# Performance work log

Measured on AMD Instinct MI355X. Metric: run time of the kernel, lower is better.

Reference implementation:

```python
import jax, jax.numpy as jnp
import numpy as np

N_EMBD = 1024
HEAD_SIZE = 64
B, T = 8, 2048


def setup_inputs() -> dict:
    key = jax.random.key(0)
    k1, k2, k3, k4 = jax.random.split(key, 4)
    scale = 1.0 / np.sqrt(N_EMBD)
    return {
        "x": jax.random.normal(k1, (B, T, N_EMBD), dtype=jnp.float32),
        "Wq": jax.random.normal(k2, (N_EMBD, HEAD_SIZE), dtype=jnp.float32) * scale,
        "Wk": jax.random.normal(k3, (N_EMBD, HEAD_SIZE), dtype=jnp.float32) * scale,
        "Wv": jax.random.normal(k4, (N_EMBD, HEAD_SIZE), dtype=jnp.float32) * scale,
    }


def reference(x, Wq, Wk, Wv):
    # x: [B, T, C]; projections (no bias)
    q = jnp.einsum("btc,ch->bth", x, Wq)
    k = jnp.einsum("btc,ch->bth", x, Wk)
    v = jnp.einsum("btc,ch->bth", x, Wv)
    head_size = k.shape[-1]
    # scaled scores [B, T, T]
    wei = jnp.einsum("bth,bsh->bts", q, k) * (head_size ** -0.5)
    # causal mask (lower-triangular keeps)
    Tlen = x.shape[1]
    causal = jnp.tril(jnp.ones((Tlen, Tlen), dtype=bool))
    wei = jnp.where(causal[None, :, :], wei, -jnp.inf)
    wei = jax.nn.softmax(wei, axis=-1)
    # dropout p=0 (eval) -> identity
    out = jnp.einsum("bts,bsh->bth", wei, v)
    return out
```

## Files before the change

### kernel.cpp

```cpp
#include <hip/hip_runtime.h>
#include <hip/hip_bf16.h>
#include <math.h>

#define Bn 8
#define Tn 2048
#define Cn 1024
#define Hn 64

typedef __attribute__((ext_vector_type(8))) short short8;
typedef __attribute__((ext_vector_type(4))) float floatx4;

#define ATTN_SCALE 0.18033688011112042f

__device__ inline unsigned short f2bf(float f) {
    union { float f; unsigned int u; } x; x.f = f;
    unsigned int r = x.u + 0x7fffu + ((x.u >> 16) & 1u);
    return (unsigned short)(r >> 16);
}

__device__ inline uint2 pack4bf(float4 v) {
    __hip_bfloat162 lo = __float22bfloat162_rn(make_float2(v.x, v.y));
    __hip_bfloat162 hi = __float22bfloat162_rn(make_float2(v.z, v.w));
    uint2 r;
    r.x = *reinterpret_cast<unsigned int*>(&lo);
    r.y = *reinterpret_cast<unsigned int*>(&hi);
    return r;
}

__device__ inline float rsum16(float v) {
    v += __shfl_xor(v, 1);
    v += __shfl_xor(v, 2);
    v += __shfl_xor(v, 4);
    v += __shfl_xor(v, 8);
    return v;
}

__global__ __launch_bounds__(256) void prep_w(
    const float* __restrict__ Wq, const float* __restrict__ Wk,
    const float* __restrict__ Wv, unsigned short* __restrict__ Wfrag)
{
    const int gid = blockIdx.x * 256 + threadIdx.x;
    const int c    = gid >> 11;
    const int rem  = gid & 2047;
    const int ks   = rem >> 6;
    const int lane = rem & 63;
    const int ln = lane & 15, qd = lane >> 4;
    const int mat = c >> 2, nc = c & 3;
    const float* W = (mat == 0) ? Wq : (mat == 1) ? Wk : Wv;
    const float sc = (mat == 0) ? ATTN_SCALE : 1.0f;
    const int col = nc * 16 + ln;
    unsigned short o[8];
    #pragma unroll
    for (int j = 0; j < 8; ++j)
        o[j] = f2bf(W[(size_t)(ks * 32 + qd * 8 + j) * Hn + col] * sc);
    *reinterpret_cast<short8*>(Wfrag + (size_t)gid * 8) = *reinterpret_cast<short8*>(o);
}

__global__ __launch_bounds__(256, 4) void proj_mfma(
    const float* __restrict__ x, const unsigned short* __restrict__ Wfrag,
    unsigned short* __restrict__ qbf, unsigned short* __restrict__ kfrag,
    unsigned short* __restrict__ vfrag)
{
    __shared__ unsigned short xs[32 * 512];

    const int ln   = threadIdx.x & 15;
    const int quad = (threadIdx.x >> 4) & 3;
    const int w    = threadIdx.x >> 6;
    const int lane = threadIdx.x & 63;
    const int row0 = blockIdx.x * 16;

    const int srow = threadIdx.x >> 4;
    const int sf   = threadIdx.x & 15;
    const float4* xrow4 = reinterpret_cast<const float4*>(x + (size_t)(row0 + srow) * Cn);

    float4 ld[16];
    #pragma unroll
    for (int it = 0; it < 16; ++it)
        ld[it] = xrow4[sf + 16 * it];
    #pragma unroll
    for (int it = 0; it < 16; ++it) {
        const int f4g = sf + 16 * it;
        const int s = f4g >> 3;
        const int q = (f4g >> 1) & 3;
        const int j = (f4g & 1) * 4;
        *reinterpret_cast<uint2*>(&xs[s * 512 + (q * 16 + srow) * 8 + j]) = pack4bf(ld[it]);
    }
    __syncthreads();

    floatx4 acc[3];
    #pragma unroll
    for (int i = 0; i < 3; ++i) acc[i] = (floatx4){0.f, 0.f, 0.f, 0.f};

    #pragma unroll 4
    for (int s = 0; s < 32; ++s) {
        const short8 a = *reinterpret_cast<const short8*>(&xs[s * 512 + lane * 8]);
        #pragma unroll
        for (int i = 0; i < 3; ++i) {
            const int cc = w * 3 + i;
            const short8 b = *reinterpret_cast<const short8*>(
                Wfrag + ((size_t)(cc * 32 + s) * 64 + lane) * 8);
            acc[i] = __builtin_amdgcn_mfma_f32_16x16x32_bf16(a, b, acc[i], 0, 0, 0);
        }
    }

    const int t0   = row0 + quad * 4;
    const int b    = t0 >> 11;
    const int tloc = t0 & 2047;
    #pragma unroll
    for (int i = 0; i < 3; ++i) {
        const int idx = w * 3 + i;
        const int mat = idx >> 2, ch = idx & 3;
        if (mat == 0) {
            #pragma unroll
            for (int r = 0; r < 4; ++r)
                qbf[(size_t)(t0 + r) * Hn + ch * 16 + ln] = f2bf(acc[i][r]);
        } else if (mat == 1) {
            const int kc = tloc >> 4;
            const int ks = ch >> 1;
            const int lq = (ch & 1) * 2 + (ln >> 3);
            #pragma unroll
            for (int r = 0; r < 4; ++r) {
                const int lanep = (quad * 4 + r) + 16 * lq;
                kfrag[(((size_t)(b * 128 + kc) * 2 + ks) * 64 + lanep) * 8 + (ln & 7)]
                    = f2bf(acc[i][r]);
            }
        } else {
            const int kb32 = tloc >> 5;
            const int off  = t0 & 31;
            const int qd   = off >> 3;
            const int j0   = off & 7;
            const int lanep = ln + 16 * qd;
            ushort4 pk;
            pk.x = f2bf(acc[i][0]); pk.y = f2bf(acc[i][1]);
            pk.z = f2bf(acc[i][2]); pk.w = f2bf(acc[i][3]);
            *reinterpret_cast<ushort4*>(
                vfrag + (((size_t)(b * 64 + kb32) * 4 + ch) * 64 + lanep) * 8 + j0) = pk;
        }
    }
}

__global__ __launch_bounds__(256, 4) void attn_mfma(
    const unsigned short* __restrict__ qbf, const unsigned short* __restrict__ kfrag,
    const unsigned short* __restrict__ vt, float* __restrict__ out)
{
    __shared__ unsigned short p_lds[4][16 * 40];
    __shared__ float o_lds[4][16][68];
    __shared__ float l_lds[4][16];

    const int j  = blockIdx.x;
    const int b  = j & 7;
    const int ti = 127 - (j >> 3);
    const int q0 = ti * 16;

    const int ln   = threadIdx.x & 15;
    const int quad = (threadIdx.x >> 4) & 3;
    const int w    = threadIdx.x >> 6;
    const int lane = threadIdx.x & 63;

    const unsigned short* qb = qbf + (size_t)b * Tn * Hn;
    const unsigned short* Kb = kfrag + (size_t)b * 131072;
    const unsigned short* Vb = vt + (size_t)b * 131072;

    const short8 aq0 = *reinterpret_cast<const short8*>(qb + (size_t)(q0 + ln) * Hn + quad * 8);
    const short8 aq1 = *reinterpret_cast<const short8*>(qb + (size_t)(q0 + ln) * Hn + 32 + quad * 8);

    floatx4 O[4];
    #pragma unroll
    for (int c = 0; c < 4; ++c) O[c] = (floatx4){0.f, 0.f, 0.f, 0.f};
    float lp[4] = {0.f, 0.f, 0.f, 0.f};

    const int ntiles = (q0 + 47) >> 5;
    const int per    = (ntiles + 3) >> 2;
    const int beg    = w * per;
    const int end    = min(beg + per, ntiles);
    unsigned short* pP = p_lds[w];

    short8 kf[4];
    if (beg < end) {
        #pragma unroll
        for (int u = 0; u < 4; ++u)
            kf[u] = *reinterpret_cast<const short8*>(Kb + ((size_t)(beg * 4 + u)) * 512 + lane * 8);
    }

    for (int t = beg; t < end; ++t) {
        const int tn = (t + 1 < end) ? (t + 1) : t;
        short8 kn[4], vf[4];
        #pragma unroll
        for (int u = 0; u < 4; ++u) {
            kn[u] = *reinterpret_cast<const short8*>(Kb + ((size_t)(tn * 4 + u)) * 512 + lane * 8);
            vf[u] = *reinterpret_cast<const short8*>(Vb + ((size_t)(t * 4 + u)) * 512 + lane * 8);
        }

        const floatx4 z = (floatx4){0.f, 0.f, 0.f, 0.f};
        floatx4 S[2];
        #pragma unroll
        for (int s = 0; s < 2; ++s) {
            S[s] = __builtin_amdgcn_mfma_f32_16x16x32_bf16(aq0, kf[s * 2], z, 0, 0, 0);
            S[s] = __builtin_amdgcn_mfma_f32_16x16x32_bf16(aq1, kf[s * 2 + 1], S[s], 0, 0, 0);
        }

        const bool diag = (t == ntiles - 1);
        #pragma unroll
        for (int s = 0; s < 2; ++s) {
            #pragma unroll
            for (int r = 0; r < 4; ++r) {
                float sv = S[s][r];
                if (diag && (t * 32 + s * 16 + ln > q0 + quad * 4 + r)) sv = -1e30f;
                const unsigned int pu = __float_as_uint(exp2f(sv));
                lp[r] += __uint_as_float(pu & 0xffff0000u);
                pP[(quad * 4 + r) * 40 + s * 16 + ln] = (unsigned short)(pu >> 16);
            }
        }
        __asm__ volatile("s_waitcnt lgkmcnt(0)" ::: "memory");
        const short8 pa = *reinterpret_cast<const short8*>(pP + ln * 40 + quad * 8);
        #pragma unroll
        for (int c = 0; c < 4; ++c)
            O[c] = __builtin_amdgcn_mfma_f32_16x16x32_bf16(pa, vf[c], O[c], 0, 0, 0);
        #pragma unroll
        for (int u = 0; u < 4; ++u) kf[u] = kn[u];
    }

    #pragma unroll
    for (int c = 0; c < 4; ++c)
        #pragma unroll
        for (int r = 0; r < 4; ++r)
            o_lds[w][quad * 4 + r][c * 16 + ln] = O[c][r];
    #pragma unroll
    for (int r = 0; r < 4; ++r) {
        const float ls = rsum16(lp[r]);
        if (ln == 0) l_lds[w][quad * 4 + r] = ls;
    }
    __syncthreads();

    const int qq = threadIdx.x >> 4;
    const int dg = threadIdx.x & 15;
    const float ltot = l_lds[0][qq] + l_lds[1][qq] + l_lds[2][qq] + l_lds[3][qq];
    const float inv = 1.0f / ltot;
    const float4 a0 = *reinterpret_cast<float4*>(&o_lds[0][qq][dg * 4]);
    const float4 a1 = *reinterpret_cast<float4*>(&o_lds[1][qq][dg * 4]);
    const float4 a2 = *reinterpret_cast<float4*>(&o_lds[2][qq][dg * 4]);
    const float4 a3 = *reinterpret_cast<float4*>(&o_lds[3][qq][dg * 4]);
    float4 r;
    r.x = (a0.x + a1.x + a2.x + a3.x) * inv;
    r.y = (a0.y + a1.y + a2.y + a3.y) * inv;
    r.z = (a0.z + a1.z + a2.z + a3.z) * inv;
    r.w = (a0.w + a1.w + a2.w + a3.w) * inv;
    *reinterpret_cast<float4*>(out + ((size_t)b * Tn + q0 + qq) * Hn + dg * 4) = r;
}

extern "C" void kernel_launch(void* const* d_in, const int* in_sizes, int n_in,
                              void* d_out, int out_size, void* d_ws, size_t ws_size,
                              hipStream_t stream) {
    (void)in_sizes; (void)n_in; (void)out_size; (void)ws_size;
    const float* x  = (const float*)d_in[0];
    const float* Wq = (const float*)d_in[1];
    const float* Wk = (const float*)d_in[2];
    const float* Wv = (const float*)d_in[3];
    float* out = (float*)d_out;

    unsigned short* Wfrag = (unsigned short*)d_ws;
    unsigned short* qbf   = Wfrag + (size_t)196608;
    unsigned short* kfr   = qbf + (size_t)Bn * Tn * Hn;
    unsigned short* vfr   = kfr + (size_t)Bn * 131072;

    prep_w<<<96, 256, 0, stream>>>(Wq, Wk, Wv, Wfrag);
    proj_mfma<<<(Bn * Tn) / 16, 256, 0, stream>>>(x, Wfrag, qbf, kfr, vfr);
    attn_mfma<<<Bn * (Tn / 16), 256, 0, stream>>>(qbf, kfr, vfr, out);
}
```

Measured before the change: 124.4 us.

## Process 32 rows per block in projection and attention to reuse K/V/W fragments

Both the projection and attention kernels now handle two 16-row tiles per block, so each loaded weight fragment and K/V fragment feeds two MFMA row tiles. The attention grid is halved and blocks are ordered by alternating long and short query tiles to balance causal work, and s_setprio is raised around the MFMA bursts. The cost is doubled accumulator registers and LDS per block, with launch bounds lowered to two blocks per CU, and fewer blocks in flight.

```diff
diff --git a/kernel.cpp b/kernel.cpp
--- a/kernel.cpp
+++ b/kernel.cpp
@@ -56,101 +56,115 @@
     *reinterpret_cast<short8*>(Wfrag + (size_t)gid * 8) = *reinterpret_cast<short8*>(o);
 }
 
-__global__ __launch_bounds__(256, 4) void proj_mfma(
+__global__ __launch_bounds__(256, 2) void proj_mfma(
     const float* __restrict__ x, const unsigned short* __restrict__ Wfrag,
     unsigned short* __restrict__ qbf, unsigned short* __restrict__ kfrag,
     unsigned short* __restrict__ vfrag)
 {
-    __shared__ unsigned short xs[32 * 512];
+    __shared__ unsigned short xs[64 * 512];
 
     const int ln   = threadIdx.x & 15;
     const int quad = (threadIdx.x >> 4) & 3;
     const int w    = threadIdx.x >> 6;
     const int lane = threadIdx.x & 63;
-    const int row0 = blockIdx.x * 16;
+    const int row0 = blockIdx.x * 32;
 
     const int srow = threadIdx.x >> 4;
     const int sf   = threadIdx.x & 15;
-    const float4* xrow4 = reinterpret_cast<const float4*>(x + (size_t)(row0 + srow) * Cn);
-
-    float4 ld[16];
-    #pragma unroll
-    for (int it = 0; it < 16; ++it)
-        ld[it] = xrow4[sf + 16 * it];
-    #pragma unroll
-    for (int it = 0; it < 16; ++it) {
-        const int f4g = sf + 16 * it;
-        const int s = f4g >> 3;
-        const int q = (f4g >> 1) & 3;
-        const int j = (f4g & 1) * 4;
-        *reinterpret_cast<uint2*>(&xs[s * 512 + (q * 16 + srow) * 8 + j]) = pack4bf(ld[it]);
+
+    #pragma unroll
+    for (int bb = 0; bb < 4; ++bb) {
+        const int row = srow + 16 * (bb >> 1);
+        const float4* xrow4 = reinterpret_cast<const float4*>(x + (size_t)(row0 + row) * Cn);
+        float4 ld[8];
+        #pragma unroll
+        for (int it = 0; it < 8; ++it)
+            ld[it] = xrow4[sf + 16 * (it + 8 * (bb & 1))];
+        const int rt = row >> 4;
+        const int rr = row & 15;
+        #pragma unroll
+        for (int it = 0; it < 8; ++it) {
+            const int f4 = sf + 16 * (it + 8 * (bb & 1));
+            const int s  = f4 >> 3;
+            const int q  = (f4 >> 1) & 3;
+            const int jj = (f4 & 1) * 4;
+            *reinterpret_cast<uint2*>(&xs[(s * 2 + rt) * 512 + (q * 16 + rr) * 8 + jj])
+                = pack4bf(ld[it]);
+        }
     }
     __syncthreads();
 
-    floatx4 acc[3];
-    #pragma unroll
-    for (int i = 0; i < 3; ++i) acc[i] = (floatx4){0.f, 0.f, 0.f, 0.f};
+    floatx4 acc[2][3];
+    #pragma unroll
+    for (int rt = 0; rt < 2; ++rt)
+        #pragma unroll
+        for (int i = 0; i < 3; ++i) acc[rt][i] = (floatx4){0.f, 0.f, 0.f, 0.f};
 
     #pragma unroll 4
     for (int s = 0; s < 32; ++s) {
-        const short8 a = *reinterpret_cast<const short8*>(&xs[s * 512 + lane * 8]);
+        const short8 a0 = *reinterpret_cast<const short8*>(&xs[(s * 2 + 0) * 512 + lane * 8]);
+        const short8 a1 = *reinterpret_cast<const short8*>(&xs[(s * 2 + 1) * 512 + lane * 8]);
         #pragma unroll
         for (int i = 0; i < 3; ++i) {
             const int cc = w * 3 + i;
             const short8 b = *reinterpret_cast<const short8*>(
                 Wfrag + ((size_t)(cc * 32 + s) * 64 + lane) * 8);
-            acc[i] = __builtin_amdgcn_mfma_f32_16x16x32_bf16(a, b, acc[i], 0, 0, 0);
-        }
-    }
-
-    const int t0   = row0 + quad * 4;
-    const int b    = t0 >> 11;
-    const int tloc = t0 & 2047;
-    #pragma unroll
-    for (int i = 0; i < 3; ++i) {
-        const int idx = w * 3 + i;
-        const int mat = idx >> 2, ch = idx & 3;
-        if (mat == 0) {
-            #pragma unroll
-            for (int r = 0; r < 4; ++r)
-                qbf[(size_t)(t0 + r) * Hn + ch * 16 + ln] = f2bf(acc[i][r]);
-        } else if (mat == 1) {
-            const int kc = tloc >> 4;
-            const int ks = ch >> 1;
-            const int lq = (ch & 1) * 2 + (ln >> 3);
-            #pragma unroll
-            for (int r = 0; r < 4; ++r) {
-                const int lanep = (quad * 4 + r) + 16 * lq;
-                kfrag[(((size_t)(b * 128 + kc) * 2 + ks) * 64 + lanep) * 8 + (ln & 7)]
-                    = f2bf(acc[i][r]);
+            acc[0][i] = __builtin_amdgcn_mfma_f32_16x16x32_bf16(a0, b, acc[0][i], 0, 0, 0);
+            acc[1][i] = __builtin_amdgcn_mfma_f32_16x16x32_bf16(a1, b, acc[1][i], 0, 0, 0);
+        }
+    }
+
+    #pragma unroll
+    for (int rt = 0; rt < 2; ++rt) {
+        const int t0   = row0 + rt * 16 + quad * 4;
+        const int b    = t0 >> 11;
+        const int tloc = t0 & 2047;
+        #pragma unroll
+        for (int i = 0; i < 3; ++i) {
+            const int idx = w * 3 + i;
+            const int mat = idx >> 2, ch = idx & 3;
+            if (mat == 0) {
+                #pragma unroll
+                for (int r = 0; r < 4; ++r)
+                    qbf[(size_t)(t0 + r) * Hn + ch * 16 + ln] = f2bf(acc[rt][i][r]);
+            } else if (mat == 1) {
+                const int kc = tloc >> 4;
+                const int ks = ch >> 1;
+                const int lq = (ch & 1) * 2 + (ln >> 3);
+                #pragma unroll
+                for (int r = 0; r < 4; ++r) {
+                    const int lanep = (quad * 4 + r) + 16 * lq;
+                    kfrag[(((size_t)(b * 128 + kc) * 2 + ks) * 64 + lanep) * 8 + (ln & 7)]
+                        = f2bf(acc[rt][i][r]);
+                }
+            } else {
+                const int kb32 = tloc >> 5;
+                const int off  = t0 & 31;
+                const int qd   = off >> 3;
+                const int j0   = off & 7;
+                const int lanep = ln + 16 * qd;
+                ushort4 pk;
+                pk.x = f2bf(acc[rt][i][0]); pk.y = f2bf(acc[rt][i][1]);
+                pk.z = f2bf(acc[rt][i][2]); pk.w = f2bf(acc[rt][i][3]);
+                *reinterpret_cast<ushort4*>(
+                    vfrag + (((size_t)(b * 64 + kb32) * 4 + ch) * 64 + lanep) * 8 + j0) = pk;
             }
-        } else {
-            const int kb32 = tloc >> 5;
-            const int off  = t0 & 31;
-            const int qd   = off >> 3;
-            const int j0   = off & 7;
-            const int lanep = ln + 16 * qd;
-            ushort4 pk;
-            pk.x = f2bf(acc[i][0]); pk.y = f2bf(acc[i][1]);
-            pk.z = f2bf(acc[i][2]); pk.w = f2bf(acc[i][3]);
-            *reinterpret_cast<ushort4*>(
-                vfrag + (((size_t)(b * 64 + kb32) * 4 + ch) * 64 + lanep) * 8 + j0) = pk;
-        }
-    }
-}
-
-__global__ __launch_bounds__(256, 4) void attn_mfma(
+        }
+    }
+}
+
+__global__ __launch_bounds__(256, 2) void attn_mfma(
     const unsigned short* __restrict__ qbf, const unsigned short* __restrict__ kfrag,
     const unsigned short* __restrict__ vt, float* __restrict__ out)
 {
-    __shared__ unsigned short p_lds[4][16 * 40];
-    __shared__ float o_lds[4][16][68];
-    __shared__ float l_lds[4][16];
+    __shared__ float osm[4][32][68];
+    __shared__ float l_lds[4][32];
 
     const int j  = blockIdx.x;
     const int b  = j & 7;
-    const int ti = 127 - (j >> 3);
-    const int q0 = ti * 16;
+    const int jj = j >> 3;
+    const int ti = (jj < 32) ? (63 - 2 * jj) : (2 * jj - 64);
+    const int q0 = ti * 32;
 
     const int ln   = threadIdx.x & 15;
     const int quad = (threadIdx.x >> 4) & 3;
@@ -161,19 +175,27 @@
     const unsigned short* Kb = kfrag + (size_t)b * 131072;
     const unsigned short* Vb = vt + (size_t)b * 131072;
 
-    const short8 aq0 = *reinterpret_cast<const short8*>(qb + (size_t)(q0 + ln) * Hn + quad * 8);
-    const short8 aq1 = *reinterpret_cast<const short8*>(qb + (size_t)(q0 + ln) * Hn + 32 + quad * 8);
-
-    floatx4 O[4];
-    #pragma unroll
-    for (int c = 0; c < 4; ++c) O[c] = (floatx4){0.f, 0.f, 0.f, 0.f};
-    float lp[4] = {0.f, 0.f, 0.f, 0.f};
-
-    const int ntiles = (q0 + 47) >> 5;
+    short8 aq[2][2];
+    #pragma unroll
+    for (int rt = 0; rt < 2; ++rt) {
+        aq[rt][0] = *reinterpret_cast<const short8*>(
+            qb + (size_t)(q0 + rt * 16 + ln) * Hn + quad * 8);
+        aq[rt][1] = *reinterpret_cast<const short8*>(
+            qb + (size_t)(q0 + rt * 16 + ln) * Hn + 32 + quad * 8);
+    }
+
+    floatx4 O[2][4];
+    #pragma unroll
+    for (int rt = 0; rt < 2; ++rt)
+        #pragma unroll
+        for (int c = 0; c < 4; ++c) O[rt][c] = (floatx4){0.f, 0.f, 0.f, 0.f};
+    float lp[2][4] = {{0.f, 0.f, 0.f, 0.f}, {0.f, 0.f, 0.f, 0.f}};
+
+    const int ntiles = ti + 1;
     const int per    = (ntiles + 3) >> 2;
     const int beg    = w * per;
     const int end    = min(beg + per, ntiles);
-    unsigned short* pP = p_lds[w];
+    unsigned short* pP = reinterpret_cast<unsigned short*>(&osm[w][0][0]);
 
     short8 kf[4];
     if (beg < end) {
@@ -192,60 +214,84 @@
         }
 
         const floatx4 z = (floatx4){0.f, 0.f, 0.f, 0.f};
-        floatx4 S[2];
-        #pragma unroll
-        for (int s = 0; s < 2; ++s) {
-            S[s] = __builtin_amdgcn_mfma_f32_16x16x32_bf16(aq0, kf[s * 2], z, 0, 0, 0);
-            S[s] = __builtin_amdgcn_mfma_f32_16x16x32_bf16(aq1, kf[s * 2 + 1], S[s], 0, 0, 0);
-        }
-
-        const bool diag = (t == ntiles - 1);
+        floatx4 S[2][2];
+        __builtin_amdgcn_s_setprio(1);
         #pragma unroll
         for (int s = 0; s < 2; ++s) {
             #pragma unroll
-            for (int r = 0; r < 4; ++r) {
-                float sv = S[s][r];
-                if (diag && (t * 32 + s * 16 + ln > q0 + quad * 4 + r)) sv = -1e30f;
-                const unsigned int pu = __float_as_uint(exp2f(sv));
-                lp[r] += __uint_as_float(pu & 0xffff0000u);
-                pP[(quad * 4 + r) * 40 + s * 16 + ln] = (unsigned short)(pu >> 16);
+            for (int rt = 0; rt < 2; ++rt) {
+                S[rt][s] = __builtin_amdgcn_mfma_f32_16x16x32_bf16(aq[rt][0], kf[s * 2], z, 0, 0, 0);
+                S[rt][s] = __builtin_amdgcn_mfma_f32_16x16x32_bf16(aq[rt][1], kf[s * 2 + 1], S[rt][s], 0, 0, 0);
             }
         }
+        __builtin_amdgcn_s_setprio(0);
+
+        const bool diag = (t == ntiles - 1);
+        #pragma unroll
+        for (int rt = 0; rt < 2; ++rt) {
+            #pragma unroll
+            for (int s = 0; s < 2; ++s) {
+                #pragma unroll
+                for (int r = 0; r < 4; ++r) {
+                    float sv = S[rt][s][r];
+                    if (diag && (t * 32 + s * 16 + ln > q0 + rt * 16 + quad * 4 + r)) sv = -1e30f;
+                    const unsigned int pu = __float_as_uint(exp2f(sv));
+                    lp[rt][r] += __uint_as_float(pu & 0xffff0000u);
+                    pP[(rt * 16 + quad * 4 + r) * 40 + s * 16 + ln] = (unsigned short)(pu >> 16);
+                }
+            }
+        }
         __asm__ volatile("s_waitcnt lgkmcnt(0)" ::: "memory");
-        const short8 pa = *reinterpret_cast<const short8*>(pP + ln * 40 + quad * 8);
+        short8 pa[2];
+        #pragma unroll
+        for (int rt = 0; rt < 2; ++rt)
+            pa[rt] = *reinterpret_cast<const short8*>(pP + (rt * 16 + ln) * 40 + quad * 8);
+        __builtin_amdgcn_s_setprio(1);
+        #pragma unroll
+        for (int rt = 0; rt < 2; ++rt)
+            #pragma unroll
+            for (int c = 0; c < 4; ++c)
+                O[rt][c] = __builtin_amdgcn_mfma_f32_16x16x32_bf16(pa[rt], vf[c], O[rt][c], 0, 0, 0);
+        __builtin_amdgcn_s_setprio(0);
+        #pragma unroll
+        for (int u = 0; u < 4; ++u) kf[u] = kn[u];
+    }
+
+    #pragma unroll
+    for (int rt = 0; rt < 2; ++rt)
         #pragma unroll
         for (int c = 0; c < 4; ++c)
-            O[c] = __builtin_amdgcn_mfma_f32_16x16x32_bf16(pa, vf[c], O[c], 0, 0, 0);
-        #pragma unroll
-        for (int u = 0; u < 4; ++u) kf[u] = kn[u];
-    }
-
-    #pragma unroll
-    for (int c = 0; c < 4; ++c)
-        #pragma unroll
-        for (int r = 0; r < 4; ++r)
-            o_lds[w][quad * 4 + r][c * 16 + ln] = O[c][r];
-    #pragma unroll
-    for (int r = 0; r < 4; ++r) {
-        const float ls = rsum16(lp[r]);
-        if (ln == 0) l_lds[w][quad * 4 + r] = ls;
-    }
+            #pragma unroll
+            for (int r = 0; r < 4; ++r)
+                osm[w][rt * 16 + quad * 4 + r][c * 16 + ln] = O[rt][c][r];
+    #pragma unroll
+    for (int rt = 0; rt < 2; ++rt)
+        #pragma unroll
+        for (int r = 0; r < 4; ++r) {
+            const float ls = rsum16(lp[rt][r]);
+            if (ln == 0) l_lds[w][rt * 16 + quad * 4 + r] = ls;
+        }
     __syncthreads();
 
-    const int qq = threadIdx.x >> 4;
-    const int dg = threadIdx.x & 15;
+    const int qq = threadIdx.x >> 3;
+    const int dg = threadIdx.x & 7;
     const float ltot = l_lds[0][qq] + l_lds[1][qq] + l_lds[2][qq] + l_lds[3][qq];
     const float inv = 1.0f / ltot;
-    const float4 a0 = *reinterpret_cast<float4*>(&o_lds[0][qq][dg * 4]);
-    const float4 a1 = *reinterpret_cast<float4*>(&o_lds[1][qq][dg * 4]);
-    const float4 a2 = *reinterpret_cast<float4*>(&o_lds[2][qq][dg * 4]);
-    const float4 a3 = *reinterpret_cast<float4*>(&o_lds[3][qq][dg * 4]);
-    float4 r;
-    r.x = (a0.x + a1.x + a2.x + a3.x) * inv;
-    r.y = (a0.y + a1.y + a2.y + a3.y) * inv;
-    r.z = (a0.z + a1.z + a2.z + a3.z) * inv;
-    r.w = (a0.w + a1.w + a2.w + a3.w) * inv;
-    *reinterpret_cast<float4*>(out + ((size_t)b * Tn + q0 + qq) * Hn + dg * 4) = r;
+    float* op = out + ((size_t)b * Tn + q0 + qq) * Hn + dg * 8;
+    #pragma unroll
+    for (int half = 0; half < 2; ++half) {
+        const int d0 = dg * 8 + half * 4;
+        const float4 a0 = *reinterpret_cast<const float4*>(&osm[0][qq][d0]);
+        const float4 a1 = *reinterpret_cast<const float4*>(&osm[1][qq][d0]);
+        const float4 a2 = *reinterpret_cast<const float4*>(&osm[2][qq][d0]);
+        const float4 a3 = *reinterpret_cast<const float4*>(&osm[3][qq][d0]);
+        float4 r;
+        r.x = (a0.x + a1.x + a2.x + a3.x) * inv;
+        r.y = (a0.y + a1.y + a2.y + a3.y) * inv;
+        r.z = (a0.z + a1.z + a2.z + a3.z) * inv;
+        r.w = (a0.w + a1.w + a2.w + a3.w) * inv;
+        *reinterpret_cast<float4*>(op + half * 4) = r;
+    }
 }
 
 extern "C" void kernel_launch(void* const* d_in, const int* in_sizes, int n_in,
@@ -264,6 +310,6 @@
     unsigned short* vfr   = kfr + (size_t)Bn * 131072;
 
     prep_w<<<96, 256, 0, stream>>>(Wq, Wk, Wv, Wfrag);
-    proj_mfma<<<(Bn * Tn) / 16, 256, 0, stream>>>(x, Wfrag, qbf, kfr, vfr);
-    attn_mfma<<<Bn * (Tn / 16), 256, 0, stream>>>(qbf, kfr, vfr, out);
-}
+    proj_mfma<<<(Bn * Tn) / 32, 256, 0, stream>>>(x, Wfrag, qbf, kfr, vfr);
+    attn_mfma<<<Bn * (Tn / 32), 256, 0, stream>>>(qbf, kfr, vfr, out);
+}
```

Result: no change. 125.8 us (+1.1%).
